# Performance work log

Hardware: AMD Instinct MI355X
Metric: run time of the kernel (lower is better)

Reference implementation:

```python
import jax, jax.numpy as jnp
import numpy as np

HID = 256   # hidden_size
NH = 8      # n_heads
DH = HID // NH  # head dim = 32
NV = 20     # num_variables
B, T = 32, 512
EPS = 1e-5


def _ln(x, g, b):
    mu = jnp.mean(x, axis=-1, keepdims=True)
    var = jnp.mean(jnp.square(x - mu), axis=-1, keepdims=True)
    return (x - mu) * jax.lax.rsqrt(var + EPS) * g + b


def setup_inputs() -> dict:
    key = jax.random.key(0)
    ks = jax.random.split(key, 20)
    s = 0.05  # xavier-ish scale for random weights
    return {
        "x": jax.random.normal(ks[0], (B, T, NV, HID), dtype=jnp.float32),
        "cls_token": jax.random.normal(ks[1], (HID,), dtype=jnp.float32) * s,
        "wq": jax.random.normal(ks[2], (HID, HID), dtype=jnp.float32) * s,
        "bq": jnp.zeros((HID,), jnp.float32),
        "wk": jax.random.normal(ks[3], (HID, HID), dtype=jnp.float32) * s,
        "bk": jnp.zeros((HID,), jnp.float32),
        "wv": jax.random.normal(ks[4], (HID, HID), dtype=jnp.float32) * s,
        "bv": jnp.zeros((HID,), jnp.float32),
        "wo": jax.random.normal(ks[5], (HID, HID), dtype=jnp.float32) * s,
        "bo": jnp.zeros((HID,), jnp.float32),
        "ln1_g": jnp.ones((HID,), jnp.float32),
        "ln1_b": jnp.zeros((HID,), jnp.float32),
        "w1": jax.random.normal(ks[6], (HID, 4 * HID), dtype=jnp.float32) * s,
        "b1": jnp.zeros((4 * HID,), jnp.float32),
        "w2": jax.random.normal(ks[7], (4 * HID, HID), dtype=jnp.float32) * s,
        "b2": jnp.zeros((HID,), jnp.float32),
        "ln2_g": jnp.ones((HID,), jnp.float32),
        "ln2_b": jnp.zeros((HID,), jnp.float32),
        "ww": jax.random.normal(ks[8], (HID, NV), dtype=jnp.float32) * s,
        "bw": jnp.zeros((NV,), jnp.float32),
    }


def reference(x, cls_token, wq, bq, wk, bk, wv, bv, wo, bo,
              ln1_g, ln1_b, w1, b1, w2, b2, ln2_g, ln2_b, ww, bw):
    # x: [B, T, V, H] -- stacked pre-projected variables (input_size == hidden_size,
    # so the torch module has no per-variable projections).
    b, t = x.shape[0], x.shape[1]
    scale = 1.0 / np.sqrt(DH)

    # Cross-attention: query = cls token (len 1), keys/values = variables (len V).
    # No static_context, so the query is shared across (b, t).
    q = (cls_token @ wq + bq).reshape(NH, DH)            # [H] -> [nh, dh]
    k = (x @ wk + bk).reshape(b, t, NV, NH, DH)          # [B,T,V,nh,dh]
    v = (x @ wv + bv).reshape(b, t, NV, NH, DH)
    scores = jnp.einsum('hd,btvhd->bthv', q, k) * scale  # [B,T,nh,V]
    attn = jax.nn.softmax(scores, axis=-1)
    ctx = jnp.einsum('bthv,btvhd->bthd', attn, v).reshape(b, t, HID)
    attn_out = ctx @ wo + bo                             # [B,T,H]

    # FF block: LN -> Linear(4H) -> GELU -> Linear(H) -> LN (dropout is eval no-op)
    h = _ln(attn_out, ln1_g, ln1_b)
    h = jax.nn.gelu(h @ w1 + b1, approximate=False)
    h = h @ w2 + b2
    processed = _ln(h, ln2_g, ln2_b)                     # [B,T,H]

    weights = jax.nn.softmax(processed @ ww + bw, axis=-1)   # [B,T,V]
    vs_output = jnp.einsum('btv,btvh->bth', weights, x)      # [B,T,H]
    return vs_output, weights
```

## Files before the change

### kernel.cpp

```cpp
#include <hip/hip_runtime.h>
#include <hip/hip_bf16.h>
#include <math.h>

#define BT   16384
#define HIDS 256
#define NHS  8
#define NVS  20

typedef __attribute__((ext_vector_type(8))) short short8;
typedef __attribute__((ext_vector_type(4))) float floatx4;

__device__ __forceinline__ float bf2f(unsigned int u) {
    union { unsigned int u; float f; } cv; cv.u = u << 16; return cv.f;
}
__device__ __forceinline__ unsigned short f2bf(float f) {
    union { __hip_bfloat16 h; unsigned short u; } cv; cv.h = __float2bfloat16(f); return cv.u;
}
__device__ __forceinline__ unsigned int pk2(float a, float b) {
    return (unsigned int)f2bf(a) | ((unsigned int)f2bf(b) << 16);
}
__device__ __forceinline__ void gload16(const void* g, void* l) {
    __builtin_amdgcn_global_load_lds(
        (const __attribute__((address_space(1))) unsigned int*)g,
        (__attribute__((address_space(3))) unsigned int*)l, 16, 0, 0);
}

__global__ __launch_bounds__(256) void k_fold(
        const float* __restrict__ cls, const float* __restrict__ wq,
        const float* __restrict__ bq, const float* __restrict__ wk,
        const float* __restrict__ bk, unsigned short* __restrict__ qkbT,
        float* __restrict__ qb) {
    __shared__ float s_q[HIDS];
    int tid = threadIdx.x;
    float acc = bq[tid];
    for (int c = 0; c < HIDS; ++c) acc += cls[c] * wq[c * HIDS + tid];
    s_q[tid] = acc;
    __syncthreads();
    int c = tid;
    #pragma unroll
    for (int h = 0; h < NHS; ++h) {
        float a = 0.f;
        #pragma unroll
        for (int d = 0; d < 32; ++d) a += wk[c * HIDS + h * 32 + d] * s_q[h * 32 + d];
        qkbT[h * HIDS + c] = f2bf(a);
    }
    #pragma unroll
    for (int h = NHS; h < 16; ++h) qkbT[h * HIDS + c] = 0;
    if (tid < NHS) {
        float a = 0.f;
        #pragma unroll
        for (int d = 0; d < 32; ++d) a += bk[tid * 32 + d] * s_q[tid * 32 + d];
        qb[tid] = a;
    }
}

__global__ __launch_bounds__(256) void k_bvo(
        const float* __restrict__ bv, const float* __restrict__ wo,
        const float* __restrict__ bo, float* __restrict__ bvo) {
    int j = threadIdx.x;
    float a = bo[j];
    for (int i = 0; i < HIDS; ++i) a += bv[i] * wo[i * HIDS + j];
    bvo[j] = a;
}

__global__ __launch_bounds__(256) void k_wvo(
        const float* __restrict__ wv, const float* __restrict__ wo,
        unsigned short* __restrict__ wvo_t) {
    int h = blockIdx.x >> 2;
    int j0 = (blockIdx.x & 3) * 64;
    int tid = threadIdx.x;
    __shared__ float s_wo[32][64];
    #pragma unroll
    for (int i = 0; i < 8; ++i) {
        int idx = i * 256 + tid;
        int d = idx >> 6, jj = idx & 63;
        s_wo[d][jj] = wo[(h * 32 + d) * HIDS + j0 + jj];
    }
    float av[32];
    #pragma unroll
    for (int d4 = 0; d4 < 8; ++d4) {
        float4 f = *(const float4*)(wv + (size_t)tid * HIDS + h * 32 + d4 * 4);
        av[d4 * 4] = f.x; av[d4 * 4 + 1] = f.y;
        av[d4 * 4 + 2] = f.z; av[d4 * 4 + 3] = f.w;
    }
    __syncthreads();
    #pragma unroll 4
    for (int jj = 0; jj < 64; ++jj) {
        float a = 0.f;
        #pragma unroll
        for (int d = 0; d < 32; ++d) a += av[d] * s_wo[d][jj];
        wvo_t[(size_t)(j0 + jj) * 2048 + h * 256 + tid] = f2bf(a);
    }
}

__global__ __launch_bounds__(256) void k_transp(const float* __restrict__ in,
        unsigned short* __restrict__ out, int R, int C) {
    __shared__ float s[32][36];
    int tid = threadIdx.x;
    int ct = blockIdx.x * 32, rt = blockIdx.y * 32;
    int r = tid >> 3, c4 = (tid & 7) * 4;
    float4 f = *(const float4*)&in[(size_t)(rt + r) * C + ct + c4];
    s[r][c4] = f.x; s[r][c4 + 1] = f.y; s[r][c4 + 2] = f.z; s[r][c4 + 3] = f.w;
    __syncthreads();
    int ro = tid >> 3, k4 = (tid & 7) * 4;
    ushort4 o;
    o.x = f2bf(s[k4][ro]);     o.y = f2bf(s[k4 + 1][ro]);
    o.z = f2bf(s[k4 + 2][ro]); o.w = f2bf(s[k4 + 3][ro]);
    *(ushort4*)&out[(size_t)(ct + ro) * R + rt + k4] = o;
}

__global__ __launch_bounds__(256) void k_attn(
        const float* __restrict__ x, const unsigned short* __restrict__ qkbT,
        const float* __restrict__ qb, unsigned short* __restrict__ xmix) {
    __shared__ __align__(16) unsigned short sX[92 * 256];
    __shared__ float s_at[4][NVS][NHS];
    int tid = threadIdx.x;
    int wave = tid >> 6, lane = tid & 63;
    int m = lane & 15, g = lane >> 4;
    size_t t0 = (size_t)blockIdx.x * 4;

    short8 qf[8];
    #pragma unroll
    for (int kk = 0; kk < 8; ++kk)
        qf[kk] = *(const short8*)&qkbT[m * HIDS + kk * 32 + g * 8];

    const float* xg = x + t0 * (NVS * HIDS);
    #pragma unroll
    for (int i = 0; i < 10; ++i) {
        int s = i * 256 + tid;
        int row = s >> 5, cc = s & 31;
        float4 f0 = *(const float4*)(xg + s * 8);
        float4 f1 = *(const float4*)(xg + s * 8 + 4);
        uint4 pk;
        pk.x = pk2(f0.x, f0.y); pk.y = pk2(f0.z, f0.w);
        pk.z = pk2(f1.x, f1.y); pk.w = pk2(f1.z, f1.w);
        int c = cc ^ (row & 7);
        *(uint4*)&sX[row * 256 + c * 8] = pk;
    }
    __syncthreads();

    int rbase = wave * NVS;
    floatx4 sc0 = {0.f, 0.f, 0.f, 0.f}, sc1 = {0.f, 0.f, 0.f, 0.f};
    #pragma unroll
    for (int kk = 0; kk < 8; ++kk) {
        int r0 = rbase + m;
        int c0 = (kk * 4 + g) ^ (r0 & 7);
        short8 a0 = *(const short8*)&sX[r0 * 256 + c0 * 8];
        int r1 = rbase + 16 + m;
        int c1 = (kk * 4 + g) ^ (r1 & 7);
        short8 a1 = *(const short8*)&sX[r1 * 256 + c1 * 8];
        sc0 = __builtin_amdgcn_mfma_f32_16x16x32_bf16(a0, qf[kk], sc0, 0, 0, 0);
        sc1 = __builtin_amdgcn_mfma_f32_16x16x32_bf16(a1, qf[kk], sc1, 0, 0, 0);
    }
    if (m < NHS) {
        #pragma unroll
        for (int r = 0; r < 4; ++r) s_at[wave][g * 4 + r][m] = sc0[r];
        if (g == 0) {
            #pragma unroll
            for (int r = 0; r < 4; ++r) s_at[wave][16 + r][m] = sc1[r];
        }
    }
    __syncthreads();

    if (lane < NHS) {
        float qbh = qb[lane];
        float sv[NVS]; float mx = -1e30f;
        #pragma unroll
        for (int v = 0; v < NVS; ++v) {
            float sc = (s_at[wave][v][lane] + qbh) * 0.17677669529663687f;
            sv[v] = sc; mx = fmaxf(mx, sc);
        }
        float sum = 0.f;
        #pragma unroll
        for (int v = 0; v < NVS; ++v) { sv[v] = expf(sv[v] - mx); sum += sv[v]; }
        float inv = 1.f / sum;
        #pragma unroll
        for (int v = 0; v < NVS; ++v) s_at[wave][v][lane] = sv[v] * inv;
    }
    __syncthreads();

    floatx4 acc[NHS];
    #pragma unroll
    for (int h = 0; h < NHS; ++h) acc[h] = (floatx4){0.f, 0.f, 0.f, 0.f};
    #pragma unroll
    for (int v = 0; v < NVS; ++v) {
        int r = rbase + v;
        int cidx = (((lane >> 1) ^ (r & 7)) << 3) + ((lane & 1) << 2);
        uint2 u = *(const uint2*)&sX[r * 256 + cidx];
        float x0 = bf2f(u.x & 0xffffu), x1 = bf2f(u.x >> 16);
        float x2 = bf2f(u.y & 0xffffu), x3 = bf2f(u.y >> 16);
        float4 w0 = *(const float4*)&s_at[wave][v][0];
        float4 w1 = *(const float4*)&s_at[wave][v][4];
        float wv8[8] = {w0.x, w0.y, w0.z, w0.w, w1.x, w1.y, w1.z, w1.w};
        #pragma unroll
        for (int h = 0; h < NHS; ++h) {
            acc[h][0] += wv8[h] * x0; acc[h][1] += wv8[h] * x1;
            acc[h][2] += wv8[h] * x2; acc[h][3] += wv8[h] * x3;
        }
    }
    unsigned short* op = xmix + (t0 + wave) * 2048;
    #pragma unroll
    for (int h = 0; h < NHS; ++h) {
        uint2 o; o.x = pk2(acc[h][0], acc[h][1]); o.y = pk2(acc[h][2], acc[h][3]);
        *(uint2*)&op[h * 256 + lane * 4] = o;
    }
}

template <int K, int NTOT, bool GELU, bool LN, bool OUTF32>
__global__ __launch_bounds__(256) void k_mg(
        const unsigned short* __restrict__ A,
        const unsigned short* __restrict__ Bt,
        const float* __restrict__ bias,
        const float* __restrict__ lng, const float* __restrict__ lnb,
        void* __restrict__ outp) {
    constexpr int BM = 32, BK = 64;
    __shared__ __align__(16) unsigned short sA[BM * BK];
    __shared__ __align__(16) unsigned short sB[256 * BK];
    __shared__ float s_sum[4][BM], s_sq[4][BM], s_ms[BM][2];
    int tid = threadIdx.x;
    int wave = tid >> 6, lane = tid & 63;
    int m = lane & 15, g = lane >> 4;
    int wn = wave * 64;
    size_t t0 = (size_t)blockIdx.x * BM;
    int n0 = blockIdx.y * 256;

    floatx4 acc[2][4];
    #pragma unroll
    for (int i = 0; i < 2; ++i)
        #pragma unroll
        for (int j = 0; j < 4; ++j) acc[i][j] = (floatx4){0.f, 0.f, 0.f, 0.f};

    for (int k0 = 0; k0 < K; k0 += BK) {
        __syncthreads();
        {
            int s = tid;
            int row = s >> 3, cc = s & 7;
            int gc = cc ^ (row & 7);
            gload16(A + (t0 + row) * K + k0 + gc * 8, (char*)sA + s * 16);
        }
        #pragma unroll
        for (int i = 0; i < 8; ++i) {
            int s = i * 256 + tid;
            int row = s >> 3, cc = s & 7;
            int gc = cc ^ (row & 7);
            gload16(Bt + (size_t)(n0 + row) * K + k0 + gc * 8, (char*)sB + s * 16);
        }
        __syncthreads();
        #pragma unroll
        for (int kk = 0; kk < 2; ++kk) {
            short8 af[2]; short8 bfr[4];
            #pragma unroll
            for (int i = 0; i < 2; ++i) {
                int row = i * 16 + m;
                int c = (kk * 4 + g) ^ (row & 7);
                af[i] = *(const short8*)&sA[row * BK + c * 8];
            }
            #pragma unroll
            for (int j = 0; j < 4; ++j) {
                int row = wn + j * 16 + m;
                int c = (kk * 4 + g) ^ (row & 7);
                bfr[j] = *(const short8*)&sB[row * BK + c * 8];
            }
            #pragma unroll
            for (int i = 0; i < 2; ++i)
                #pragma unroll
                for (int j = 0; j < 4; ++j)
                    acc[i][j] = __builtin_amdgcn_mfma_f32_16x16x32_bf16(af[i], bfr[j], acc[i][j], 0, 0, 0);
        }
    }

    float vv[2][4][4];
    #pragma unroll
    for (int j = 0; j < 4; ++j) {
        float bj = bias[n0 + wn + j * 16 + m];
        #pragma unroll
        for (int i = 0; i < 2; ++i)
            #pragma unroll
            for (int r = 0; r < 4; ++r) {
                float v = acc[i][j][r] + bj;
                if (GELU) v = 0.5f * v * (1.f + erff(v * 0.70710678118654752f));
                vv[i][j][r] = v;
            }
    }

    if (LN) {
        float ps[2][4], pq[2][4];
        #pragma unroll
        for (int i = 0; i < 2; ++i)
            #pragma unroll
            for (int r = 0; r < 4; ++r) {
                float s = 0.f, q = 0.f;
                #pragma unroll
                for (int j = 0; j < 4; ++j) { float v = vv[i][j][r]; s += v; q += v * v; }
                #pragma unroll
                for (int mk = 1; mk < 16; mk <<= 1) {
                    s += __shfl_xor(s, mk, 64);
                    q += __shfl_xor(q, mk, 64);
                }
                ps[i][r] = s; pq[i][r] = q;
            }
        if ((lane & 15) == 0) {
            #pragma unroll
            for (int i = 0; i < 2; ++i)
                #pragma unroll
                for (int r = 0; r < 4; ++r) {
                    int row = i * 16 + g * 4 + r;
                    s_sum[wave][row] = ps[i][r];
                    s_sq[wave][row] = pq[i][r];
                }
        }
        __syncthreads();
        if (tid < BM) {
            float ts = 0.f, tq = 0.f;
            #pragma unroll
            for (int w = 0; w < 4; ++w) { ts += s_sum[w][tid]; tq += s_sq[w][tid]; }
            float mean = ts * (1.f / 256.f);
            float var = tq * (1.f / 256.f) - mean * mean;
            s_ms[tid][0] = mean; s_ms[tid][1] = rsqrtf(var + 1e-5f);
        }
        __syncthreads();
        float lg[4], lb[4];
        #pragma unroll
        for (int j = 0; j < 4; ++j) {
            lg[j] = lng[wn + j * 16 + m];
            lb[j] = lnb[wn + j * 16 + m];
        }
        #pragma unroll
        for (int i = 0; i < 2; ++i)
            #pragma unroll
            for (int r = 0; r < 4; ++r) {
                int row = i * 16 + g * 4 + r;
                float mean = s_ms[row][0], rstd = s_ms[row][1];
                #pragma unroll
                for (int j = 0; j < 4; ++j)
                    vv[i][j][r] = (vv[i][j][r] - mean) * rstd * lg[j] + lb[j];
            }
    }

    #pragma unroll
    for (int i = 0; i < 2; ++i)
        #pragma unroll
        for (int r = 0; r < 4; ++r) {
            size_t grow = t0 + i * 16 + g * 4 + r;
            #pragma unroll
            for (int j = 0; j < 4; ++j) {
                float v = vv[i][j][r];
                if (OUTF32) {
                    ((float*)outp)[grow * NTOT + n0 + wn + j * 16 + m] = v;
                } else {
                    float v2 = __shfl_xor(v, 1);
                    if (!(lane & 1))
                        *(unsigned int*)((unsigned short*)outp + grow * NTOT + n0 + wn + j * 16 + m) = pk2(v, v2);
                }
            }
        }
}

__global__ __launch_bounds__(256) void k_wsel(
        const float* __restrict__ in, const float* __restrict__ lng,
        const float* __restrict__ lnb, const float* __restrict__ ww,
        const float* __restrict__ bw, const float* __restrict__ x,
        float* __restrict__ wout, float* __restrict__ vs_out) {
    __shared__ float s_p[16][HIDS + 1];
    __shared__ float s_red[2][16][16];
    __shared__ float s_ms[16][2];
    __shared__ float s_lg[16][NVS];
    __shared__ float s_w[16][NVS];
    int tid = threadIdx.x;
    size_t t0 = (size_t)blockIdx.x * 16;
    #pragma unroll
    for (int i = 0; i < 4; ++i) {
        int idx4 = i * 256 + tid;
        float4 f = ((const float4*)(in + t0 * HIDS))[idx4];
        int flat = idx4 * 4;
        int r = flat >> 8, c = flat & 255;
        s_p[r][c] = f.x; s_p[r][c + 1] = f.y; s_p[r][c + 2] = f.z; s_p[r][c + 3] = f.w;
    }
    __syncthreads();
    int r = tid >> 4, jg = tid & 15;
    float sum = 0.f, sq = 0.f;
    #pragma unroll
    for (int i = 0; i < 16; ++i) {
        float a = s_p[r][jg * 16 + i]; sum += a; sq += a * a;
    }
    s_red[0][r][jg] = sum; s_red[1][r][jg] = sq;
    __syncthreads();
    if (jg == 0) {
        float ts = 0.f, tq = 0.f;
        #pragma unroll
        for (int i = 0; i < 16; ++i) { ts += s_red[0][r][i]; tq += s_red[1][r][i]; }
        float mean = ts * (1.f / HIDS);
        float var = tq * (1.f / HIDS) - mean * mean;
        s_ms[r][0] = mean; s_ms[r][1] = rsqrtf(var + 1e-5f);
    }
    __syncthreads();
    float mean = s_ms[r][0], rstd = s_ms[r][1];
    #pragma unroll
    for (int i = 0; i < 16; ++i) {
        int c = jg * 16 + i;
        s_p[r][c] = (s_p[r][c] - mean) * rstd * lng[c] + lnb[c];
    }
    __syncthreads();
    if (jg < 10) {
        int o = jg * 2;
        float a0 = bw[o], a1 = bw[o + 1];
        #pragma unroll 4
        for (int c = 0; c < HIDS; ++c) {
            float a = s_p[r][c];
            const float2 w = *(const float2*)(ww + c * NVS + o);
            a0 += a * w.x; a1 += a * w.y;
        }
        s_lg[r][o] = a0; s_lg[r][o + 1] = a1;
    }
    __syncthreads();
    if (tid < 16) {
        int rr = tid;
        float mx = -1e30f;
        #pragma unroll
        for (int v = 0; v < NVS; ++v) mx = fmaxf(mx, s_lg[rr][v]);
        float e[NVS]; float ssum = 0.f;
        #pragma unroll
        for (int v = 0; v < NVS; ++v) { e[v] = expf(s_lg[rr][v] - mx); ssum += e[v]; }
        float inv = 1.f / ssum;
        #pragma unroll
        for (int v = 0; v < NVS; ++v) {
            float wv_ = e[v] * inv;
            s_w[rr][v] = wv_;
            wout[(t0 + rr) * NVS + v] = wv_;
        }
    }
    __syncthreads();
    int wave = tid >> 6, l = tid & 63;
    #pragma unroll
    for (int tt = 0; tt < 4; ++tt) {
        int t = wave * 4 + tt;
        const float4* xt = (const float4*)(x + (t0 + t) * (NVS * HIDS));
        float4 acc = make_float4(0.f, 0.f, 0.f, 0.f);
        #pragma unroll
        for (int v = 0; v < NVS; ++v) {
            float w = s_w[t][v];
            float4 a = xt[v * 64 + l];
            acc.x += w * a.x; acc.y += w * a.y; acc.z += w * a.z; acc.w += w * a.w;
        }
        ((float4*)(vs_out + (t0 + t) * HIDS))[l] = acc;
    }
}

extern "C" void kernel_launch(void* const* d_in, const int* in_sizes, int n_in,
                              void* d_out, int out_size, void* d_ws, size_t ws_size,
                              hipStream_t stream) {
    const float* x     = (const float*)d_in[0];
    const float* cls   = (const float*)d_in[1];
    const float* wq    = (const float*)d_in[2];
    const float* bq    = (const float*)d_in[3];
    const float* wk    = (const float*)d_in[4];
    const float* bk    = (const float*)d_in[5];
    const float* wv    = (const float*)d_in[6];
    const float* bv    = (const float*)d_in[7];
    const float* wo    = (const float*)d_in[8];
    const float* bo    = (const float*)d_in[9];
    const float* ln1_g = (const float*)d_in[10];
    const float* ln1_b = (const float*)d_in[11];
    const float* w1    = (const float*)d_in[12];
    const float* b1    = (const float*)d_in[13];
    const float* w2    = (const float*)d_in[14];
    const float* b2    = (const float*)d_in[15];
    const float* ln2_g = (const float*)d_in[16];
    const float* ln2_b = (const float*)d_in[17];
    const float* ww    = (const float*)d_in[18];
    const float* bw    = (const float*)d_in[19];

    float* outf   = (float*)d_out;
    float* vs_out = outf;
    float* w_out  = outf + (size_t)BT * HIDS;

    char* ws = (char*)d_ws;
    unsigned short* qkbT = (unsigned short*)ws;
    float* qb   = (float*)(ws + 8192);
    float* bvo  = (float*)(ws + 8448);
    unsigned short* w1t   = (unsigned short*)(ws + 16384);
    unsigned short* w2t   = (unsigned short*)(ws + 16384 + 524288);
    unsigned short* wvo_t = (unsigned short*)(ws + 16384 + 1048576);
    char* big = ws + 16384 + 1048576 + 1048576;
    unsigned short* bufA = (unsigned short*)big;
    unsigned short* hb   = (unsigned short*)(big + (size_t)BT * 2048 * 2);
    float* buf1 = (float*)(big + (size_t)BT * 2048 * 2 + (size_t)BT * HIDS * 2);

    k_fold<<<1, 256, 0, stream>>>(cls, wq, bq, wk, bk, qkbT, qb);
    k_bvo<<<1, 256, 0, stream>>>(bv, wo, bo, bvo);
    k_wvo<<<32, 256, 0, stream>>>(wv, wo, wvo_t);
    k_transp<<<dim3(32, 8), 256, 0, stream>>>(w1, w1t, 256, 1024);
    k_transp<<<dim3(8, 32), 256, 0, stream>>>(w2, w2t, 1024, 256);

    k_attn<<<BT / 4, 256, 0, stream>>>(x, qkbT, qb, bufA);
    k_mg<2048, 256, false, true, false><<<dim3(BT / 32, 1), 256, 0, stream>>>(
        bufA, wvo_t, bvo, ln1_g, ln1_b, hb);
    k_mg<256, 1024, true, false, false><<<dim3(BT / 32, 4), 256, 0, stream>>>(
        hb, w1t, b1, nullptr, nullptr, bufA);
    k_mg<1024, 256, false, false, true><<<dim3(BT / 32, 1), 256, 0, stream>>>(
        bufA, w2t, b2, nullptr, nullptr, buf1);
    k_wsel<<<BT / 16, 256, 0, stream>>>(buf1, ln2_g, ln2_b, ww, bw, x, w_out, vs_out);
}
```

Before: 742.8 us.

## Fuse Wvo GEMM, LN1, FFN, LN2 and variable selection into one kernel

Replaces the three k_mg GEMM launches and the k_wsel kernel with a single k_ff kernel per 32-row tile. LN1 output and the GELU hidden chunks stay in swizzled LDS, so the hidden activations (hb, the 1024-wide FFN buffer, the fp32 buf1) are no longer round-tripped through global memory. The FFN is processed in four 256-column chunks whose results accumulate straight into the second GEMM, and the selection logits and softmax run in the same block. In exchange the block uses about 76KB of LDS, which lowers occupancy, and the k_attn shared buffer is also shrunk.

```diff
diff --git a/kernel.cpp b/kernel.cpp
--- a/kernel.cpp
+++ b/kernel.cpp
@@ -112,7 +112,7 @@
 __global__ __launch_bounds__(256) void k_attn(
         const float* __restrict__ x, const unsigned short* __restrict__ qkbT,
         const float* __restrict__ qb, unsigned short* __restrict__ xmix) {
-    __shared__ __align__(16) unsigned short sX[92 * 256];
+    __shared__ __align__(16) unsigned short sX[80 * 256];
     __shared__ float s_at[4][NVS][NHS];
     int tid = threadIdx.x;
     int wave = tid >> 6, lane = tid & 63;
@@ -206,85 +206,89 @@
     }
 }
 
-template <int K, int NTOT, bool GELU, bool LN, bool OUTF32>
-__global__ __launch_bounds__(256) void k_mg(
-        const unsigned short* __restrict__ A,
-        const unsigned short* __restrict__ Bt,
-        const float* __restrict__ bias,
-        const float* __restrict__ lng, const float* __restrict__ lnb,
-        void* __restrict__ outp) {
-    constexpr int BM = 32, BK = 64;
-    __shared__ __align__(16) unsigned short sA[BM * BK];
-    __shared__ __align__(16) unsigned short sB[256 * BK];
-    __shared__ float s_sum[4][BM], s_sq[4][BM], s_ms[BM][2];
+__global__ __launch_bounds__(256) void k_ff(
+        const unsigned short* __restrict__ xmix,
+        const unsigned short* __restrict__ wvo_t,
+        const float* __restrict__ bvo,
+        const float* __restrict__ ln1g, const float* __restrict__ ln1b,
+        const unsigned short* __restrict__ w1t,
+        const float* __restrict__ b1,
+        const unsigned short* __restrict__ w2t,
+        const float* __restrict__ b2,
+        const float* __restrict__ ln2g, const float* __restrict__ ln2b,
+        const float* __restrict__ ww, const float* __restrict__ bw,
+        const float* __restrict__ x,
+        float* __restrict__ w_out, float* __restrict__ vs_out) {
+    __shared__ __align__(16) char smem[76032];
+    unsigned short* sB  = (unsigned short*)smem;
+    unsigned short* sA  = (unsigned short*)(smem + 32768);
+    unsigned short* sH  = (unsigned short*)(smem + 36864);
+    unsigned short* sH1 = (unsigned short*)(smem + 53248);
+    float* sP    = (float*)(smem + 36864);
+    float* s_sum = (float*)(smem + 69632);
+    float* s_sq  = (float*)(smem + 70144);
+    float* s_ms  = (float*)(smem + 70656);
+    float* s_lg  = (float*)(smem + 70912);
+    float* s_w   = (float*)(smem + 73472);
+    float* s_ww  = (float*)smem;
+
     int tid = threadIdx.x;
     int wave = tid >> 6, lane = tid & 63;
     int m = lane & 15, g = lane >> 4;
     int wn = wave * 64;
-    size_t t0 = (size_t)blockIdx.x * BM;
-    int n0 = blockIdx.y * 256;
-
-    floatx4 acc[2][4];
+    size_t t0 = (size_t)blockIdx.x * 32;
+
+    floatx4 accA[2][4], acc3[2][4];
     #pragma unroll
     for (int i = 0; i < 2; ++i)
         #pragma unroll
-        for (int j = 0; j < 4; ++j) acc[i][j] = (floatx4){0.f, 0.f, 0.f, 0.f};
-
-    for (int k0 = 0; k0 < K; k0 += BK) {
+        for (int j = 0; j < 4; ++j) {
+            accA[i][j] = (floatx4){0.f, 0.f, 0.f, 0.f};
+            acc3[i][j] = (floatx4){0.f, 0.f, 0.f, 0.f};
+        }
+
+    for (int k0 = 0; k0 < 2048; k0 += 64) {
         __syncthreads();
         {
-            int s = tid;
-            int row = s >> 3, cc = s & 7;
-            int gc = cc ^ (row & 7);
-            gload16(A + (t0 + row) * K + k0 + gc * 8, (char*)sA + s * 16);
-        }
-        #pragma unroll
-        for (int i = 0; i < 8; ++i) {
-            int s = i * 256 + tid;
-            int row = s >> 3, cc = s & 7;
-            int gc = cc ^ (row & 7);
-            gload16(Bt + (size_t)(n0 + row) * K + k0 + gc * 8, (char*)sB + s * 16);
+            int s = tid, row = s >> 3, cc = s & 7, gc = cc ^ (row & 7);
+            gload16(xmix + (t0 + row) * 2048 + k0 + gc * 8, (char*)sA + s * 16);
+        }
+        #pragma unroll
+        for (int p = 0; p < 8; ++p) {
+            int s = p * 256 + tid, row = s >> 3, cc = s & 7, gc = cc ^ (row & 7);
+            gload16(wvo_t + (size_t)row * 2048 + k0 + gc * 8, (char*)sB + s * 16);
         }
         __syncthreads();
         #pragma unroll
         for (int kk = 0; kk < 2; ++kk) {
-            short8 af[2]; short8 bfr[4];
+            short8 af[2], bf[4];
             #pragma unroll
             for (int i = 0; i < 2; ++i) {
-                int row = i * 16 + m;
-                int c = (kk * 4 + g) ^ (row & 7);
-                af[i] = *(const short8*)&sA[row * BK + c * 8];
+                int row = i * 16 + m, c = (kk * 4 + g) ^ (row & 7);
+                af[i] = *(const short8*)&sA[row * 64 + c * 8];
             }
             #pragma unroll
             for (int j = 0; j < 4; ++j) {
-                int row = wn + j * 16 + m;
-                int c = (kk * 4 + g) ^ (row & 7);
-                bfr[j] = *(const short8*)&sB[row * BK + c * 8];
+                int row = wn + j * 16 + m, c = (kk * 4 + g) ^ (row & 7);
+                bf[j] = *(const short8*)&sB[row * 64 + c * 8];
             }
             #pragma unroll
             for (int i = 0; i < 2; ++i)
                 #pragma unroll
                 for (int j = 0; j < 4; ++j)
-                    acc[i][j] = __builtin_amdgcn_mfma_f32_16x16x32_bf16(af[i], bfr[j], acc[i][j], 0, 0, 0);
-        }
-    }
-
-    float vv[2][4][4];
-    #pragma unroll
-    for (int j = 0; j < 4; ++j) {
-        float bj = bias[n0 + wn + j * 16 + m];
-        #pragma unroll
-        for (int i = 0; i < 2; ++i)
-            #pragma unroll
-            for (int r = 0; r < 4; ++r) {
-                float v = acc[i][j][r] + bj;
-                if (GELU) v = 0.5f * v * (1.f + erff(v * 0.70710678118654752f));
-                vv[i][j][r] = v;
-            }
-    }
-
-    if (LN) {
-        float ps[2][4], pq[2][4];
+                    accA[i][j] = __builtin_amdgcn_mfma_f32_16x16x32_bf16(af[i], bf[j], accA[i][j], 0, 0, 0);
+        }
+    }
+    {
+        float vv[2][4][4];
+        #pragma unroll
+        for (int j = 0; j < 4; ++j) {
+            float bj = bvo[wn + j * 16 + m];
+            #pragma unroll
+            for (int i = 0; i < 2; ++i)
+                #pragma unroll
+                for (int r = 0; r < 4; ++r) vv[i][j][r] = accA[i][j][r] + bj;
+        }
         #pragma unroll
         for (int i = 0; i < 2; ++i)
             #pragma unroll
@@ -297,152 +301,240 @@
                     s += __shfl_xor(s, mk, 64);
                     q += __shfl_xor(q, mk, 64);
                 }
-                ps[i][r] = s; pq[i][r] = q;
-            }
-        if ((lane & 15) == 0) {
-            #pragma unroll
-            for (int i = 0; i < 2; ++i)
-                #pragma unroll
-                for (int r = 0; r < 4; ++r) {
+                if ((lane & 15) == 0) {
                     int row = i * 16 + g * 4 + r;
-                    s_sum[wave][row] = ps[i][r];
-                    s_sq[wave][row] = pq[i][r];
-                }
-        }
-        __syncthreads();
-        if (tid < BM) {
+                    s_sum[wave * 32 + row] = s;
+                    s_sq[wave * 32 + row] = q;
+                }
+            }
+        __syncthreads();
+        if (tid < 32) {
             float ts = 0.f, tq = 0.f;
             #pragma unroll
-            for (int w = 0; w < 4; ++w) { ts += s_sum[w][tid]; tq += s_sq[w][tid]; }
+            for (int w = 0; w < 4; ++w) { ts += s_sum[w * 32 + tid]; tq += s_sq[w * 32 + tid]; }
             float mean = ts * (1.f / 256.f);
             float var = tq * (1.f / 256.f) - mean * mean;
-            s_ms[tid][0] = mean; s_ms[tid][1] = rsqrtf(var + 1e-5f);
-        }
-        __syncthreads();
-        float lg[4], lb[4];
+            s_ms[tid * 2] = mean; s_ms[tid * 2 + 1] = rsqrtf(var + 1e-5f);
+        }
+        __syncthreads();
+        float lg_[4], lb_[4];
         #pragma unroll
         for (int j = 0; j < 4; ++j) {
-            lg[j] = lng[wn + j * 16 + m];
-            lb[j] = lnb[wn + j * 16 + m];
+            lg_[j] = ln1g[wn + j * 16 + m];
+            lb_[j] = ln1b[wn + j * 16 + m];
         }
         #pragma unroll
         for (int i = 0; i < 2; ++i)
             #pragma unroll
             for (int r = 0; r < 4; ++r) {
                 int row = i * 16 + g * 4 + r;
-                float mean = s_ms[row][0], rstd = s_ms[row][1];
-                #pragma unroll
-                for (int j = 0; j < 4; ++j)
-                    vv[i][j][r] = (vv[i][j][r] - mean) * rstd * lg[j] + lb[j];
-            }
-    }
-
-    #pragma unroll
-    for (int i = 0; i < 2; ++i)
-        #pragma unroll
-        for (int r = 0; r < 4; ++r) {
-            size_t grow = t0 + i * 16 + g * 4 + r;
-            #pragma unroll
-            for (int j = 0; j < 4; ++j) {
-                float v = vv[i][j][r];
-                if (OUTF32) {
-                    ((float*)outp)[grow * NTOT + n0 + wn + j * 16 + m] = v;
-                } else {
+                float mean = s_ms[row * 2], rstd = s_ms[row * 2 + 1];
+                #pragma unroll
+                for (int j = 0; j < 4; ++j) {
+                    float v = (vv[i][j][r] - mean) * rstd * lg_[j] + lb_[j];
                     float v2 = __shfl_xor(v, 1);
-                    if (!(lane & 1))
-                        *(unsigned int*)((unsigned short*)outp + grow * NTOT + n0 + wn + j * 16 + m) = pk2(v, v2);
-                }
-            }
-        }
-}
-
-__global__ __launch_bounds__(256) void k_wsel(
-        const float* __restrict__ in, const float* __restrict__ lng,
-        const float* __restrict__ lnb, const float* __restrict__ ww,
-        const float* __restrict__ bw, const float* __restrict__ x,
-        float* __restrict__ wout, float* __restrict__ vs_out) {
-    __shared__ float s_p[16][HIDS + 1];
-    __shared__ float s_red[2][16][16];
-    __shared__ float s_ms[16][2];
-    __shared__ float s_lg[16][NVS];
-    __shared__ float s_w[16][NVS];
-    int tid = threadIdx.x;
-    size_t t0 = (size_t)blockIdx.x * 16;
-    #pragma unroll
-    for (int i = 0; i < 4; ++i) {
-        int idx4 = i * 256 + tid;
-        float4 f = ((const float4*)(in + t0 * HIDS))[idx4];
-        int flat = idx4 * 4;
-        int r = flat >> 8, c = flat & 255;
-        s_p[r][c] = f.x; s_p[r][c + 1] = f.y; s_p[r][c + 2] = f.z; s_p[r][c + 3] = f.w;
-    }
-    __syncthreads();
-    int r = tid >> 4, jg = tid & 15;
-    float sum = 0.f, sq = 0.f;
-    #pragma unroll
-    for (int i = 0; i < 16; ++i) {
-        float a = s_p[r][jg * 16 + i]; sum += a; sq += a * a;
-    }
-    s_red[0][r][jg] = sum; s_red[1][r][jg] = sq;
-    __syncthreads();
-    if (jg == 0) {
-        float ts = 0.f, tq = 0.f;
-        #pragma unroll
-        for (int i = 0; i < 16; ++i) { ts += s_red[0][r][i]; tq += s_red[1][r][i]; }
-        float mean = ts * (1.f / HIDS);
-        float var = tq * (1.f / HIDS) - mean * mean;
-        s_ms[r][0] = mean; s_ms[r][1] = rsqrtf(var + 1e-5f);
-    }
-    __syncthreads();
-    float mean = s_ms[r][0], rstd = s_ms[r][1];
-    #pragma unroll
-    for (int i = 0; i < 16; ++i) {
-        int c = jg * 16 + i;
-        s_p[r][c] = (s_p[r][c] - mean) * rstd * lng[c] + lnb[c];
-    }
-    __syncthreads();
-    if (jg < 10) {
-        int o = jg * 2;
-        float a0 = bw[o], a1 = bw[o + 1];
+                    if (!(lane & 1)) {
+                        int colE = wn + j * 16 + m;
+                        int chunk = colE >> 3;
+                        int lc = ((chunk ^ (row & 7)) << 3) + (colE & 7);
+                        *(unsigned int*)&sH[row * 256 + lc] = pk2(v, v2);
+                    }
+                }
+            }
+    }
+
+    for (int nc = 0; nc < 4; ++nc) {
+        #pragma unroll
+        for (int i = 0; i < 2; ++i)
+            #pragma unroll
+            for (int j = 0; j < 4; ++j) accA[i][j] = (floatx4){0.f, 0.f, 0.f, 0.f};
+        for (int k0 = 0; k0 < 256; k0 += 64) {
+            __syncthreads();
+            #pragma unroll
+            for (int p = 0; p < 8; ++p) {
+                int s = p * 256 + tid, row = s >> 3, cc = s & 7, gc = cc ^ (row & 7);
+                gload16(w1t + (size_t)(nc * 256 + row) * 256 + k0 + gc * 8, (char*)sB + s * 16);
+            }
+            __syncthreads();
+            #pragma unroll
+            for (int kk = 0; kk < 2; ++kk) {
+                short8 af[2], bf[4];
+                #pragma unroll
+                for (int i = 0; i < 2; ++i) {
+                    int row = i * 16 + m;
+                    int c = (k0 >> 3) + ((kk * 4 + g) ^ (row & 7));
+                    af[i] = *(const short8*)&sH[row * 256 + c * 8];
+                }
+                #pragma unroll
+                for (int j = 0; j < 4; ++j) {
+                    int row = wn + j * 16 + m, c = (kk * 4 + g) ^ (row & 7);
+                    bf[j] = *(const short8*)&sB[row * 64 + c * 8];
+                }
+                #pragma unroll
+                for (int i = 0; i < 2; ++i)
+                    #pragma unroll
+                    for (int j = 0; j < 4; ++j)
+                        accA[i][j] = __builtin_amdgcn_mfma_f32_16x16x32_bf16(af[i], bf[j], accA[i][j], 0, 0, 0);
+            }
+        }
+        __syncthreads();
+        #pragma unroll
+        for (int i = 0; i < 2; ++i)
+            #pragma unroll
+            for (int r = 0; r < 4; ++r) {
+                int row = i * 16 + g * 4 + r;
+                #pragma unroll
+                for (int j = 0; j < 4; ++j) {
+                    float v = accA[i][j][r] + b1[nc * 256 + wn + j * 16 + m];
+                    v = 0.5f * v * (1.f + erff(v * 0.70710678118654752f));
+                    float v2 = __shfl_xor(v, 1);
+                    if (!(lane & 1)) {
+                        int colE = wn + j * 16 + m;
+                        int chunk = colE >> 3;
+                        int lc = ((chunk ^ (row & 7)) << 3) + (colE & 7);
+                        *(unsigned int*)&sH1[row * 256 + lc] = pk2(v, v2);
+                    }
+                }
+            }
+        for (int k0 = 0; k0 < 256; k0 += 64) {
+            __syncthreads();
+            #pragma unroll
+            for (int p = 0; p < 8; ++p) {
+                int s = p * 256 + tid, row = s >> 3, cc = s & 7, gc = cc ^ (row & 7);
+                gload16(w2t + (size_t)row * 1024 + nc * 256 + k0 + gc * 8, (char*)sB + s * 16);
+            }
+            __syncthreads();
+            #pragma unroll
+            for (int kk = 0; kk < 2; ++kk) {
+                short8 af[2], bf[4];
+                #pragma unroll
+                for (int i = 0; i < 2; ++i) {
+                    int row = i * 16 + m;
+                    int c = (k0 >> 3) + ((kk * 4 + g) ^ (row & 7));
+                    af[i] = *(const short8*)&sH1[row * 256 + c * 8];
+                }
+                #pragma unroll
+                for (int j = 0; j < 4; ++j) {
+                    int row = wn + j * 16 + m, c = (kk * 4 + g) ^ (row & 7);
+                    bf[j] = *(const short8*)&sB[row * 64 + c * 8];
+                }
+                #pragma unroll
+                for (int i = 0; i < 2; ++i)
+                    #pragma unroll
+                    for (int j = 0; j < 4; ++j)
+                        acc3[i][j] = __builtin_amdgcn_mfma_f32_16x16x32_bf16(af[i], bf[j], acc3[i][j], 0, 0, 0);
+            }
+        }
+    }
+
+    {
+        float vv[2][4][4];
+        #pragma unroll
+        for (int j = 0; j < 4; ++j) {
+            float bj = b2[wn + j * 16 + m];
+            #pragma unroll
+            for (int i = 0; i < 2; ++i)
+                #pragma unroll
+                for (int r = 0; r < 4; ++r) vv[i][j][r] = acc3[i][j][r] + bj;
+        }
+        __syncthreads();
+        #pragma unroll
+        for (int i = 0; i < 2; ++i)
+            #pragma unroll
+            for (int r = 0; r < 4; ++r) {
+                float s = 0.f, q = 0.f;
+                #pragma unroll
+                for (int j = 0; j < 4; ++j) { float v = vv[i][j][r]; s += v; q += v * v; }
+                #pragma unroll
+                for (int mk = 1; mk < 16; mk <<= 1) {
+                    s += __shfl_xor(s, mk, 64);
+                    q += __shfl_xor(q, mk, 64);
+                }
+                if ((lane & 15) == 0) {
+                    int row = i * 16 + g * 4 + r;
+                    s_sum[wave * 32 + row] = s;
+                    s_sq[wave * 32 + row] = q;
+                }
+            }
+        __syncthreads();
+        if (tid < 32) {
+            float ts = 0.f, tq = 0.f;
+            #pragma unroll
+            for (int w = 0; w < 4; ++w) { ts += s_sum[w * 32 + tid]; tq += s_sq[w * 32 + tid]; }
+            float mean = ts * (1.f / 256.f);
+            float var = tq * (1.f / 256.f) - mean * mean;
+            s_ms[tid * 2] = mean; s_ms[tid * 2 + 1] = rsqrtf(var + 1e-5f);
+        }
+        __syncthreads();
+        #pragma unroll
+        for (int i = 0; i < 2; ++i)
+            #pragma unroll
+            for (int r = 0; r < 4; ++r) {
+                int row = i * 16 + g * 4 + r;
+                float mean = s_ms[row * 2], rstd = s_ms[row * 2 + 1];
+                #pragma unroll
+                for (int j = 0; j < 4; ++j) {
+                    int col = wn + j * 16 + m;
+                    float v = (vv[i][j][r] - mean) * rstd * ln2g[col] + ln2b[col];
+                    sP[row * 256 + ((col + 2 * row) & 255)] = v;
+                }
+            }
+    }
+    __syncthreads();
+
+    #pragma unroll
+    for (int p = 0; p < 20; ++p) {
+        int idx = p * 256 + tid;
+        if (idx < 5120) s_ww[idx] = ww[idx];
+    }
+    if (tid < 20) s_ww[5120 + tid] = bw[tid];
+    __syncthreads();
+
+    {
+        int row = tid >> 3, q = tid & 7;
+        float a0 = 0.f, a1 = 0.f, a2 = 0.f;
         #pragma unroll 4
-        for (int c = 0; c < HIDS; ++c) {
-            float a = s_p[r][c];
-            const float2 w = *(const float2*)(ww + c * NVS + o);
-            a0 += a * w.x; a1 += a * w.y;
-        }
-        s_lg[r][o] = a0; s_lg[r][o + 1] = a1;
-    }
-    __syncthreads();
-    if (tid < 16) {
-        int rr = tid;
+        for (int c = 0; c < 256; ++c) {
+            float p = sP[row * 256 + ((c + 2 * row) & 255)];
+            a0 += p * s_ww[c * 20 + q];
+            a1 += p * s_ww[c * 20 + q + 8];
+            if (q < 4) a2 += p * s_ww[c * 20 + q + 16];
+        }
+        s_lg[row * 20 + q] = a0 + s_ww[5120 + q];
+        s_lg[row * 20 + q + 8] = a1 + s_ww[5120 + q + 8];
+        if (q < 4) s_lg[row * 20 + q + 16] = a2 + s_ww[5120 + q + 16];
+    }
+    __syncthreads();
+
+    if (tid < 32) {
         float mx = -1e30f;
         #pragma unroll
-        for (int v = 0; v < NVS; ++v) mx = fmaxf(mx, s_lg[rr][v]);
+        for (int v = 0; v < NVS; ++v) mx = fmaxf(mx, s_lg[tid * 20 + v]);
         float e[NVS]; float ssum = 0.f;
         #pragma unroll
-        for (int v = 0; v < NVS; ++v) { e[v] = expf(s_lg[rr][v] - mx); ssum += e[v]; }
+        for (int v = 0; v < NVS; ++v) { e[v] = expf(s_lg[tid * 20 + v] - mx); ssum += e[v]; }
         float inv = 1.f / ssum;
         #pragma unroll
         for (int v = 0; v < NVS; ++v) {
             float wv_ = e[v] * inv;
-            s_w[rr][v] = wv_;
-            wout[(t0 + rr) * NVS + v] = wv_;
-        }
-    }
-    __syncthreads();
-    int wave = tid >> 6, l = tid & 63;
-    #pragma unroll
-    for (int tt = 0; tt < 4; ++tt) {
-        int t = wave * 4 + tt;
-        const float4* xt = (const float4*)(x + (t0 + t) * (NVS * HIDS));
+            s_w[tid * 20 + v] = wv_;
+            w_out[(t0 + tid) * NVS + v] = wv_;
+        }
+    }
+    __syncthreads();
+
+    #pragma unroll
+    for (int tt = 0; tt < 8; ++tt) {
+        int row = wave * 8 + tt;
+        const float4* xt = (const float4*)(x + (t0 + row) * (size_t)(NVS * HIDS));
         float4 acc = make_float4(0.f, 0.f, 0.f, 0.f);
         #pragma unroll
         for (int v = 0; v < NVS; ++v) {
-            float w = s_w[t][v];
-            float4 a = xt[v * 64 + l];
+            float w = s_w[row * 20 + v];
+            float4 a = xt[v * 64 + lane];
             acc.x += w * a.x; acc.y += w * a.y; acc.z += w * a.z; acc.w += w * a.w;
         }
-        ((float4*)(vs_out + (t0 + t) * HIDS))[l] = acc;
+        ((float4*)(vs_out + (t0 + row) * HIDS))[lane] = acc;
     }
 }
 
@@ -481,10 +573,7 @@
     unsigned short* w1t   = (unsigned short*)(ws + 16384);
     unsigned short* w2t   = (unsigned short*)(ws + 16384 + 524288);
     unsigned short* wvo_t = (unsigned short*)(ws + 16384 + 1048576);
-    char* big = ws + 16384 + 1048576 + 1048576;
-    unsigned short* bufA = (unsigned short*)big;
-    unsigned short* hb   = (unsigned short*)(big + (size_t)BT * 2048 * 2);
-    float* buf1 = (float*)(big + (size_t)BT * 2048 * 2 + (size_t)BT * HIDS * 2);
+    unsigned short* bufA  = (unsigned short*)(ws + 16384 + 2097152);
 
     k_fold<<<1, 256, 0, stream>>>(cls, wq, bq, wk, bk, qkbT, qb);
     k_bvo<<<1, 256, 0, stream>>>(bv, wo, bo, bvo);
@@ -493,11 +582,7 @@
     k_transp<<<dim3(8, 32), 256, 0, stream>>>(w2, w2t, 1024, 256);
 
     k_attn<<<BT / 4, 256, 0, stream>>>(x, qkbT, qb, bufA);
-    k_mg<2048, 256, false, true, false><<<dim3(BT / 32, 1), 256, 0, stream>>>(
-        bufA, wvo_t, bvo, ln1_g, ln1_b, hb);
-    k_mg<256, 1024, true, false, false><<<dim3(BT / 32, 4), 256, 0, stream>>>(
-        hb, w1t, b1, nullptr, nullptr, bufA);
-    k_mg<1024, 256, false, false, true><<<dim3(BT / 32, 1), 256, 0, stream>>>(
-        bufA, w2t, b2, nullptr, nullptr, buf1);
-    k_wsel<<<BT / 16, 256, 0, stream>>>(buf1, ln2_g, ln2_b, ww, bw, x, w_out, vs_out);
-}
+    k_ff<<<BT / 32, 256, 0, stream>>>(bufA, wvo_t, bvo, ln1_g, ln1_b,
+                                      w1t, b1, w2t, b2, ln2_g, ln2_b,
+                                      ww, bw, x, w_out, vs_out);
+}
```

Result: faster. 725.9 us (-2.3%).
